# Kernel optimization log

Measured on AMD Instinct MI355X. Metric: run time of the kernel, lower is better.

## Reference

```python
import jax, jax.numpy as jnp
import numpy as np

EMBED_DIM = 512
NUM_HEADS = 8
HEAD_DIM = EMBED_DIM // NUM_HEADS
EDGE_HIDDEN = 512
B, L = 2, 512


def setup_inputs() -> dict:
    key = jax.random.key(0)
    ks = jax.random.split(key, 16)
    s = 0.02
    inp = {
        "query": jax.random.normal(ks[0], (B, L, EMBED_DIM), jnp.float32),
        "key_in": jax.random.normal(ks[1], (B, L, EMBED_DIM), jnp.float32),
        "value": jax.random.normal(ks[2], (B, L, EMBED_DIM), jnp.float32),
        "edge_representation": jax.random.normal(ks[3], (B, L, L), jnp.float32),
        # projection weights stored as [in, out]: y = x @ W + b
        "Wq": jax.random.normal(ks[4], (EMBED_DIM, EMBED_DIM), jnp.float32) * s,
        "bq": jnp.zeros((EMBED_DIM,), jnp.float32),
        "Wk": jax.random.normal(ks[5], (EMBED_DIM, EMBED_DIM), jnp.float32) * s,
        "bk": jnp.zeros((EMBED_DIM,), jnp.float32),
        "Wv": jax.random.normal(ks[6], (EMBED_DIM, EMBED_DIM), jnp.float32) * s,
        "bv": jnp.zeros((EMBED_DIM,), jnp.float32),
        "Wo": jax.random.normal(ks[7], (EMBED_DIM, EMBED_DIM), jnp.float32) * s,
        "bo": jnp.zeros((EMBED_DIM,), jnp.float32),
        # edge MLP: Linear(1 -> 512) -> ReLU -> Linear(512 -> num_heads)
        "We1": jax.random.normal(ks[8], (1, EDGE_HIDDEN), jnp.float32) * s,
        "be1": jnp.zeros((EDGE_HIDDEN,), jnp.float32),
        "We2": jax.random.normal(ks[9], (EDGE_HIDDEN, NUM_HEADS), jnp.float32) * s,
        "be2": jnp.zeros((NUM_HEADS,), jnp.float32),
    }
    return inp


def reference(query, key_in, value, edge_representation,
              Wq, bq, Wk, bk, Wv, bv, Wo, bo, We1, be1, We2, be2):
    Bc, Lc, _ = query.shape
    # project and split heads: [B, H, L, Dh]
    def split_heads(x):
        return x.reshape(Bc, Lc, NUM_HEADS, HEAD_DIM).transpose(0, 2, 1, 3)
    Q = split_heads(query @ Wq + bq)
    K = split_heads(key_in @ Wk + bk)
    V = split_heads(value @ Wv + bv)
    # edge MLP on scalar edge features: [B, L, L, 1] -> [B, L, L, H]
    e = edge_representation[..., None]
    h = jax.nn.relu(e * We1[0] + be1)          # [B, L, L, 512]
    edge_bias = h @ We2 + be2                   # [B, L, L, H]
    scale = 1.0 / jnp.sqrt(jnp.asarray(HEAD_DIM, query.dtype))
    scores = jnp.einsum("bhqd,bhkd->bhqk", Q, K) * scale
    scores = scores + edge_bias.transpose(0, 3, 1, 2)  # [B, H, L, L]
    attn = jax.nn.softmax(scores, axis=-1)
    out = jnp.einsum("bhqk,bhkd->bhqd", attn, V)
    out = out.transpose(0, 2, 1, 3).reshape(Bc, Lc, EMBED_DIM)
    return out @ Wo + bo
```

## Files before the change

kernel.cpp:

```cpp
#include <hip/hip_runtime.h>
#include <hip/hip_bf16.h>

typedef __attribute__((ext_vector_type(8))) short bf16x8;
typedef __attribute__((ext_vector_type(4))) float f32x4;

#define LOG2E 1.44269504088896340736f

#define XQ_OFF 0
#define XK_OFF 524288
#define XV_OFF 1048576
#define WQ_OFF 1572864
#define WK_OFF 1835008
#define WV_OFF 2097152
#define WO_OFF 2359296
#define QB_OFF 2621440
#define KB_OFF 3145728
#define VT_OFF 3670016
#define AO_OFF 4194304
#define T_B   9437184
#define A_B   (T_B + 4096)
#define C_B   (A_B + 20480)
#define SEG_B (C_B + 20480)

struct MegaArgs {
  const float *xq, *xk, *xv, *eg;
  const float *wq, *wk, *wv, *wo;
  const float *bq, *bk, *bv, *bo;
  const float *w1, *b1, *we2, *be2;
  float* out;
  unsigned short* wsb;
  float *wsT, *wsA, *wsC;
  unsigned short* segp;
};

__device__ __forceinline__ unsigned short f2bf(float f) {
  union { __hip_bfloat16 h; unsigned short u; } c;
  c.h = __float2bfloat16(f);
  return c.u;
}

__device__ void prep_block(const MegaArgs& a, char* smem) {
  float* sT   = (float*)smem;
  int*   sIdx = (int*)(smem + 2048);
  float (*sDA)[8] = (float (*)[8])(smem + 4096);
  float (*sDC)[8] = (float (*)[8])(smem + 20480);
  float* sA0 = (float*)(smem + 36864);
  float* sC0 = (float*)(smem + 36896);
  int tid = threadIdx.x;
  for (int p = tid; p < 512; p += 256) {
    float w = a.w1[p], bb = a.b1[p];
    sT[p] = (w != 0.f) ? (-bb / w) : -3.4e38f;
    sIdx[p] = p;
#pragma unroll
    for (int h = 0; h < 8; ++h) {
      float w2 = a.we2[p * 8 + h];
      float ra = 0.f, rc = 0.f;
      if (w < 0.f)       { ra = w2 * w; rc = w2 * bb; }
      else if (w == 0.f) { rc = w2 * fmaxf(bb, 0.f); }
      sDA[p][h] = ra; sDC[p][h] = rc;
    }
  }
  __syncthreads();
  for (int size = 2; size <= 512; size <<= 1) {
    for (int stride = size >> 1; stride > 0; stride >>= 1) {
      int p = tid;
      int i = ((p / stride) * (stride << 1)) + (p % stride);
      int j = i + stride;
      bool up = ((i & size) == 0);
      float ti = sT[i], tj = sT[j];
      if (up ? (ti > tj) : (ti < tj)) {
        sT[i] = tj; sT[j] = ti;
        int t = sIdx[i]; sIdx[i] = sIdx[j]; sIdx[j] = t;
      }
      __syncthreads();
    }
  }
#pragma unroll
  for (int h = 0; h < 8; ++h) { sDA[tid][h] += sDA[tid + 256][h]; sDC[tid][h] += sDC[tid + 256][h]; }
  __syncthreads();
  for (int st = 128; st > 0; st >>= 1) {
    if (tid < st) {
#pragma unroll
      for (int h = 0; h < 8; ++h) { sDA[tid][h] += sDA[tid + st][h]; sDC[tid][h] += sDC[tid + st][h]; }
    }
    __syncthreads();
  }
  if (tid < 8) { sA0[tid] = sDA[0][tid]; sC0[tid] = sDC[0][tid] + a.be2[tid]; }
  __syncthreads();
  for (int p = tid; p < 512; p += 256) {
    int k = sIdx[p];
    float wk = a.w1[k], bk2 = a.b1[k];
#pragma unroll
    for (int h = 0; h < 8; ++h) {
      float w2 = a.we2[k * 8 + h];
      float da = 0.f, dc = 0.f;
      if (wk > 0.f)      { da =  w2 * wk; dc =  w2 * bk2; }
      else if (wk < 0.f) { da = -w2 * wk; dc = -w2 * bk2; }
      sDA[p][h] = da; sDC[p][h] = dc;
    }
  }
  __syncthreads();
  for (int off = 1; off < 512; off <<= 1) {
    float ra[2][8], rc[2][8];
#pragma unroll
    for (int e = 0; e < 2; ++e) {
      int p = tid + e * 256;
      if (p >= off) {
#pragma unroll
        for (int h = 0; h < 8; ++h) { ra[e][h] = sDA[p - off][h]; rc[e][h] = sDC[p - off][h]; }
      }
    }
    __syncthreads();
#pragma unroll
    for (int e = 0; e < 2; ++e) {
      int p = tid + e * 256;
      if (p >= off) {
#pragma unroll
        for (int h = 0; h < 8; ++h) { sDA[p][h] += ra[e][h]; sDC[p][h] += rc[e][h]; }
      }
    }
    __syncthreads();
  }
  a.wsT[tid] = sT[tid]; a.wsT[tid + 256] = sT[tid + 256];
  if (tid < 8) { a.wsA[tid] = sA0[tid]; a.wsC[tid] = sC0[tid]; }
  for (int p = tid; p < 512; p += 256) {
#pragma unroll
    for (int h = 0; h < 8; ++h) {
      a.wsA[(p + 1) * 8 + h] = sA0[h] + sDA[p][h];
      a.wsC[(p + 1) * 8 + h] = sC0[h] + sDC[p][h];
    }
  }
}

__device__ void transpose2(const MegaArgs& a, int tblk, char* smem) {
  unsigned short (*sWt)[72] = (unsigned short (*)[72])smem;
  int tid = threadIdx.x;
  for (int it = 0; it < 2; ++it) {
    int t = tblk * 2 + it;
    int mat = t >> 6, tile = t & 63;
    int k0 = (tile >> 3) * 64, n0 = (tile & 7) * 64;
    const float* src = (mat == 0) ? a.wq : (mat == 1) ? a.wk : (mat == 2) ? a.wv : a.wo;
    int row = tid >> 2, cq = tid & 3;
    const float4* sp = (const float4*)(src + (size_t)(k0 + row) * 512 + n0 + cq * 16);
    if (it) __syncthreads();
#pragma unroll
    for (int j2 = 0; j2 < 4; ++j2) {
      float4 v = sp[j2];
      int nl = cq * 16 + j2 * 4;
      sWt[nl + 0][row] = f2bf(v.x);
      sWt[nl + 1][row] = f2bf(v.y);
      sWt[nl + 2][row] = f2bf(v.z);
      sWt[nl + 3][row] = f2bf(v.w);
    }
    __syncthreads();
    int n = tid >> 2, kq = tid & 3;
    unsigned short* dst = a.wsb + WQ_OFF + mat * 262144 + (size_t)(n0 + n) * 512 + k0 + kq * 16;
    *(uint4*)dst       = *(const uint4*)&sWt[n][kq * 16];
    *(uint4*)(dst + 8) = *(const uint4*)&sWt[n][kq * 16 + 8];
  }
}

__device__ void convert_units(const MegaArgs& a, int blk) {
  int tid = threadIdx.x;
  for (int u = blk - 129; u < 1536; u += 383) {
    int i = u * 256 + tid;
    int region = i >> 17, off = i & 131071;
    const float* src = (region == 0) ? a.xq : (region == 1) ? a.xk : a.xv;
    float4 v = ((const float4*)src)[off];
    ushort4 o;
    o.x = f2bf(v.x); o.y = f2bf(v.y); o.z = f2bf(v.z); o.w = f2bf(v.w);
    ((ushort4*)a.wsb)[i] = o;
  }
}

__device__ void seg_block(const MegaArgs& a, int sblk, char* smem) {
  float* sT = (float*)smem;
  int tid = threadIdx.x;
  sT[tid] = a.wsT[tid]; sT[tid + 256] = a.wsT[tid + 256];
  __syncthreads();
  int base = sblk * 4096;
  for (int j2 = 0; j2 < 16; ++j2) {
    int i = base + j2 * 256 + tid;
    float ev = a.eg[i];
    int lo = 0, hi = 512;
    while (lo < hi) {
      int mid = (lo + hi) >> 1;
      if (sT[mid] < ev) lo = mid + 1; else hi = mid;
    }
    a.segp[i] = (unsigned short)lo;
  }
}

__device__ void gemm_tile(const unsigned short* __restrict__ A, const unsigned short* __restrict__ Wt,
                          const float* __restrict__ bias, void* out, int mode,
                          int m0, int n0, char* smem) {
  const int K = 512;
  unsigned short (*sA)[72]  = (unsigned short (*)[72])smem;
  unsigned short (*sBt)[72] = (unsigned short (*)[72])(smem + 9216);
  int tid = threadIdx.x, wave = tid >> 6, lane = tid & 63;
  int quad = lane >> 4, l16 = lane & 15;
  f32x4 acc[4] = {{0.f,0.f,0.f,0.f},{0.f,0.f,0.f,0.f},{0.f,0.f,0.f,0.f},{0.f,0.f,0.f,0.f}};
  int lr = tid >> 2, ls = tid & 3;
  for (int kb = 0; kb < K; kb += 64) {
    __syncthreads();
    *(uint4*)&sA[lr][ls * 16]      = *(const uint4*)(A  + (size_t)(m0 + lr) * K + kb + ls * 16);
    *(uint4*)&sA[lr][ls * 16 + 8]  = *(const uint4*)(A  + (size_t)(m0 + lr) * K + kb + ls * 16 + 8);
    *(uint4*)&sBt[lr][ls * 16]     = *(const uint4*)(Wt + (size_t)(n0 + lr) * K + kb + ls * 16);
    *(uint4*)&sBt[lr][ls * 16 + 8] = *(const uint4*)(Wt + (size_t)(n0 + lr) * K + kb + ls * 16 + 8);
    __syncthreads();
    for (int ks = 0; ks < 2; ++ks) {
      bf16x8 af = *(const bf16x8*)&sA[wave * 16 + l16][ks * 32 + quad * 8];
#pragma unroll
      for (int nt = 0; nt < 4; ++nt) {
        bf16x8 bf = *(const bf16x8*)&sBt[nt * 16 + l16][ks * 32 + quad * 8];
        acc[nt] = __builtin_amdgcn_mfma_f32_16x16x32_bf16(af, bf, acc[nt], 0, 0, 0);
      }
    }
  }
  int mbase = m0 + wave * 16 + quad * 4;
#pragma unroll
  for (int nt = 0; nt < 4; ++nt) {
    int n = n0 + nt * 16 + l16;
    float bv = bias[n];
#pragma unroll
    for (int r = 0; r < 4; ++r) {
      float v = acc[nt][r] + bv;
      int m = mbase + r;
      if (mode == 0) {
        int b = m >> 9, l = m & 511, hh = n >> 6, d = n & 63;
        ((unsigned short*)out)[(((size_t)(b * 8 + hh) * 512) + l) * 64 + d] = f2bf(v);
      } else if (mode == 1) {
        ((float*)out)[(size_t)m * 512 + n] = v;
      } else {
        int b = m >> 9, l = m & 511, hh = n >> 6, d = n & 63;
        ((unsigned short*)out)[(((size_t)(b * 8 + hh) * 64) + d) * 512 + l] = f2bf(v);
      }
    }
  }
}

__device__ void attn_block(const MegaArgs& a, int qt, int h, int b, char* smem) {
  float* sAh = (float*)smem;
  float* sCh = (float*)(smem + 2052);
  unsigned short (*sP)[16][40] = (unsigned short (*)[16][40])(smem + 4112);
  float (*sO)[4][16][16] = (float (*)[4][16][16])(smem + 9232);
  float (*sM)[16] = (float (*)[16])(smem + 25616);
  float (*sL)[16] = (float (*)[16])(smem + 25872);
  const unsigned short* Qb = a.wsb + QB_OFF;
  const unsigned short* Kb = a.wsb + KB_OFF;
  const unsigned short* Vt = a.wsb + VT_OFF;
  int bh = b * 8 + h;
  int q0 = qt * 16;
  int tid = threadIdx.x, wave = tid >> 6, lane = tid & 63;
  int quad = lane >> 4, l16 = lane & 15;
  for (int i = tid; i < 513; i += 256) { sAh[i] = a.wsA[i * 8 + h]; sCh[i] = a.wsC[i * 8 + h]; }
  const unsigned short* qp = Qb + ((size_t)bh * 512 + q0 + l16) * 64 + quad * 8;
  bf16x8 qf0 = *(const bf16x8*)qp;
  bf16x8 qf1 = *(const bf16x8*)(qp + 32);
  int key_base = wave * 128;
  f32x4 S[4][2];
#pragma unroll
  for (int kt = 0; kt < 4; ++kt) {
    int key0 = key_base + kt * 32;
#pragma unroll
    for (int half = 0; half < 2; ++half) {
      const unsigned short* kp = Kb + ((size_t)bh * 512 + key0 + half * 16 + l16) * 64 + quad * 8;
      bf16x8 kf0 = *(const bf16x8*)kp;
      bf16x8 kf1 = *(const bf16x8*)(kp + 32);
      f32x4 acc = {0.f, 0.f, 0.f, 0.f};
      acc = __builtin_amdgcn_mfma_f32_16x16x32_bf16(qf0, kf0, acc, 0, 0, 0);
      acc = __builtin_amdgcn_mfma_f32_16x16x32_bf16(qf1, kf1, acc, 0, 0, 0);
      S[kt][half] = acc;
    }
  }
  __syncthreads();
#pragma unroll
  for (int kt = 0; kt < 4; ++kt)
#pragma unroll
    for (int half = 0; half < 2; ++half)
#pragma unroll
      for (int r = 0; r < 4; ++r) {
        int eidx = (b * 512 + q0 + quad * 4 + r) * 512 + key_base + kt * 32 + half * 16 + l16;
        float ev = a.eg[eidx];
        int sg = a.segp[eidx];
        S[kt][half][r] = S[kt][half][r] * 0.125f + sAh[sg] * ev + sCh[sg];
      }
  float m_w[4], l_w[4];
#pragma unroll
  for (int r = 0; r < 4; ++r) {
    float mx = -3.4e38f;
#pragma unroll
    for (int kt = 0; kt < 4; ++kt) { mx = fmaxf(mx, fmaxf(S[kt][0][r], S[kt][1][r])); }
    for (int off = 1; off < 16; off <<= 1) mx = fmaxf(mx, __shfl_xor(mx, off, 64));
    float s = 0.f;
#pragma unroll
    for (int kt = 0; kt < 4; ++kt)
#pragma unroll
      for (int half = 0; half < 2; ++half) {
        float p = exp2f((S[kt][half][r] - mx) * LOG2E);
        S[kt][half][r] = p; s += p;
      }
    for (int off = 1; off < 16; off <<= 1) s += __shfl_xor(s, off, 64);
    m_w[r] = mx; l_w[r] = s;
  }
  f32x4 Oacc[4] = {{0.f,0.f,0.f,0.f},{0.f,0.f,0.f,0.f},{0.f,0.f,0.f,0.f},{0.f,0.f,0.f,0.f}};
#pragma unroll
  for (int kt = 0; kt < 4; ++kt) {
    int key0 = key_base + kt * 32;
#pragma unroll
    for (int half = 0; half < 2; ++half)
#pragma unroll
      for (int r = 0; r < 4; ++r)
        sP[wave][quad * 4 + r][half * 16 + l16] = f2bf(S[kt][half][r]);
    __builtin_amdgcn_wave_barrier();
    bf16x8 pf = *(const bf16x8*)&sP[wave][l16][quad * 8];
    __builtin_amdgcn_wave_barrier();
#pragma unroll
    for (int nt = 0; nt < 4; ++nt) {
      bf16x8 vf = *(const bf16x8*)(Vt + ((size_t)bh * 64 + nt * 16 + l16) * 512 + key0 + quad * 8);
      Oacc[nt] = __builtin_amdgcn_mfma_f32_16x16x32_bf16(pf, vf, Oacc[nt], 0, 0, 0);
    }
  }
  if (l16 == 0) {
#pragma unroll
    for (int r = 0; r < 4; ++r) { sM[wave][quad * 4 + r] = m_w[r]; sL[wave][quad * 4 + r] = l_w[r]; }
  }
#pragma unroll
  for (int nt = 0; nt < 4; ++nt)
#pragma unroll
    for (int r = 0; r < 4; ++r)
      sO[wave][nt][quad * 4 + r][l16] = Oacc[nt][r];
  __syncthreads();
#pragma unroll
  for (int r = 0; r < 4; ++r) {
    int row = quad * 4 + r;
    float M = fmaxf(fmaxf(sM[0][row], sM[1][row]), fmaxf(sM[2][row], sM[3][row]));
    float L = 0.f, Ov = 0.f;
#pragma unroll
    for (int wv = 0; wv < 4; ++wv) {
      float f = exp2f((sM[wv][row] - M) * LOG2E);
      L += f * sL[wv][row];
      Ov += f * sO[wv][wave][row][l16];
    }
    float v = Ov / L;
    (a.wsb + AO_OFF)[((size_t)(b * 512 + q0 + row)) * 512 + h * 64 + wave * 16 + l16] = f2bf(v);
  }
}

__global__ __launch_bounds__(256) void k_pre(MegaArgs a) {
  __shared__ __align__(16) char smem[36928];
  int blk = blockIdx.x;
  if (blk == 0) prep_block(a, smem);
  else if (blk <= 128) transpose2(a, blk - 1, smem);
  else convert_units(a, blk);
}

__global__ __launch_bounds__(256) void k_qkv(MegaArgs a) {
  __shared__ __align__(16) char smem[18432];
  int blk = blockIdx.x;
  if (blk < 384) {
    int z = blk >> 7, rem = blk & 127;
    const unsigned short* A  = a.wsb + ((z == 0) ? XQ_OFF : (z == 1) ? XK_OFF : XV_OFF);
    const unsigned short* Wt = a.wsb + ((z == 0) ? WQ_OFF : (z == 1) ? WK_OFF : WV_OFF);
    const float* bias = (z == 0) ? a.bq : (z == 1) ? a.bk : a.bv;
    void* outp = (void*)(a.wsb + ((z == 0) ? QB_OFF : (z == 1) ? KB_OFF : VT_OFF));
    gemm_tile(A, Wt, bias, outp, (z == 2) ? 2 : 0, (rem & 15) * 64, (rem >> 4) * 64, smem);
  } else {
    seg_block(a, blk - 384, smem);
  }
}

__global__ __launch_bounds__(256) void k_at(MegaArgs a) {
  __shared__ __align__(16) char smem[26128];
  int blk = blockIdx.x;
  attn_block(a, blk & 31, (blk >> 5) & 7, blk >> 8, smem);
}

__global__ __launch_bounds__(256) void k_og(MegaArgs a) {
  __shared__ __align__(16) char smem[18432];
  gemm_tile(a.wsb + AO_OFF, a.wsb + WO_OFF, a.bo, (void*)a.out, 1,
            (blockIdx.x & 15) * 64, (blockIdx.x >> 4) * 64, smem);
}

extern "C" void kernel_launch(void* const* d_in, const int* in_sizes, int n_in,
                              void* d_out, int out_size, void* d_ws, size_t ws_size,
                              hipStream_t stream) {
  MegaArgs a;
  a.xq  = (const float*)d_in[0];
  a.xk  = (const float*)d_in[1];
  a.xv  = (const float*)d_in[2];
  a.eg  = (const float*)d_in[3];
  a.wq  = (const float*)d_in[4];
  a.bq  = (const float*)d_in[5];
  a.wk  = (const float*)d_in[6];
  a.bk  = (const float*)d_in[7];
  a.wv  = (const float*)d_in[8];
  a.bv  = (const float*)d_in[9];
  a.wo  = (const float*)d_in[10];
  a.bo  = (const float*)d_in[11];
  a.w1  = (const float*)d_in[12];
  a.b1  = (const float*)d_in[13];
  a.we2 = (const float*)d_in[14];
  a.be2 = (const float*)d_in[15];
  a.out = (float*)d_out;
  a.wsb = (unsigned short*)d_ws;
  a.wsT = (float*)((char*)d_ws + T_B);
  a.wsA = (float*)((char*)d_ws + A_B);
  a.wsC = (float*)((char*)d_ws + C_B);
  a.segp = (unsigned short*)((char*)d_ws + SEG_B);

  k_pre<<<512, 256, 0, stream>>>(a);
  k_qkv<<<512, 256, 0, stream>>>(a);
  k_at<<<512, 256, 0, stream>>>(a);
  k_og<<<128, 256, 0, stream>>>(a);
}
```

Baseline: 156.1 us.

## Spread conversion and segment search over more blocks; head-major prefix tables

The input bf16 conversion now runs one unit per block over 1536 extra blocks instead of a strided loop over 383 blocks, and the edge segment binary search uses 512 blocks of 1024 elements with a fixed 9-step branchless search instead of 128 blocks of 4096 elements. The per-head prefix tables wsA/wsC are stored head-major, so attention blocks read them contiguously instead of with a stride of 8. The aim is better latency hiding and occupancy in the pre and qkv kernels, and coalesced table loads. The cost is more block launch and scheduling overhead.

Measured after the change: 141.8 us. 1.1x faster.

```diff
diff --git a/kernel.cpp b/kernel.cpp
--- a/kernel.cpp
+++ b/kernel.cpp
@@ -122,12 +122,12 @@
     __syncthreads();
   }
   a.wsT[tid] = sT[tid]; a.wsT[tid + 256] = sT[tid + 256];
-  if (tid < 8) { a.wsA[tid] = sA0[tid]; a.wsC[tid] = sC0[tid]; }
+  if (tid < 8) { a.wsA[tid * 513] = sA0[tid]; a.wsC[tid * 513] = sC0[tid]; }
   for (int p = tid; p < 512; p += 256) {
 #pragma unroll
     for (int h = 0; h < 8; ++h) {
-      a.wsA[(p + 1) * 8 + h] = sA0[h] + sDA[p][h];
-      a.wsC[(p + 1) * 8 + h] = sC0[h] + sDC[p][h];
+      a.wsA[h * 513 + p + 1] = sA0[h] + sDA[p][h];
+      a.wsC[h * 513 + p + 1] = sC0[h] + sDC[p][h];
     }
   }
 }
@@ -160,35 +160,30 @@
   }
 }
 
-__device__ void convert_units(const MegaArgs& a, int blk) {
-  int tid = threadIdx.x;
-  for (int u = blk - 129; u < 1536; u += 383) {
-    int i = u * 256 + tid;
-    int region = i >> 17, off = i & 131071;
-    const float* src = (region == 0) ? a.xq : (region == 1) ? a.xk : a.xv;
-    float4 v = ((const float4*)src)[off];
-    ushort4 o;
-    o.x = f2bf(v.x); o.y = f2bf(v.y); o.z = f2bf(v.z); o.w = f2bf(v.w);
-    ((ushort4*)a.wsb)[i] = o;
-  }
-}
-
 __device__ void seg_block(const MegaArgs& a, int sblk, char* smem) {
   float* sT = (float*)smem;
   int tid = threadIdx.x;
   sT[tid] = a.wsT[tid]; sT[tid + 256] = a.wsT[tid + 256];
   __syncthreads();
-  int base = sblk * 4096;
-  for (int j2 = 0; j2 < 16; ++j2) {
-    int i = base + j2 * 256 + tid;
-    float ev = a.eg[i];
+  int base = sblk * 1024;
+  float ev[4];
+#pragma unroll
+  for (int j = 0; j < 4; ++j) ev[j] = a.eg[base + j * 256 + tid];
+  int res[4];
+#pragma unroll
+  for (int j = 0; j < 4; ++j) {
     int lo = 0, hi = 512;
-    while (lo < hi) {
+#pragma unroll
+    for (int it = 0; it < 9; ++it) {
       int mid = (lo + hi) >> 1;
-      if (sT[mid] < ev) lo = mid + 1; else hi = mid;
-    }
-    a.segp[i] = (unsigned short)lo;
-  }
+      bool c = sT[mid] < ev[j];
+      lo = c ? mid + 1 : lo;
+      hi = c ? hi : mid;
+    }
+    res[j] = lo;
+  }
+#pragma unroll
+  for (int j = 0; j < 4; ++j) a.segp[base + j * 256 + tid] = (unsigned short)res[j];
 }
 
 __device__ void gemm_tile(const unsigned short* __restrict__ A, const unsigned short* __restrict__ Wt,
@@ -253,7 +248,7 @@
   int q0 = qt * 16;
   int tid = threadIdx.x, wave = tid >> 6, lane = tid & 63;
   int quad = lane >> 4, l16 = lane & 15;
-  for (int i = tid; i < 513; i += 256) { sAh[i] = a.wsA[i * 8 + h]; sCh[i] = a.wsC[i * 8 + h]; }
+  for (int i = tid; i < 513; i += 256) { sAh[i] = a.wsA[h * 513 + i]; sCh[i] = a.wsC[h * 513 + i]; }
   const unsigned short* qp = Qb + ((size_t)bh * 512 + q0 + l16) * 64 + quad * 8;
   bf16x8 qf0 = *(const bf16x8*)qp;
   bf16x8 qf1 = *(const bf16x8*)(qp + 32);
@@ -352,7 +347,15 @@
   int blk = blockIdx.x;
   if (blk == 0) prep_block(a, smem);
   else if (blk <= 128) transpose2(a, blk - 1, smem);
-  else convert_units(a, blk);
+  else {
+    int i = (blk - 129) * 256 + threadIdx.x;
+    int region = i >> 17, off = i & 131071;
+    const float* src = (region == 0) ? a.xq : (region == 1) ? a.xk : a.xv;
+    float4 v = ((const float4*)src)[off];
+    ushort4 o;
+    o.x = f2bf(v.x); o.y = f2bf(v.y); o.z = f2bf(v.z); o.w = f2bf(v.w);
+    ((ushort4*)a.wsb)[i] = o;
+  }
 }
 
 __global__ __launch_bounds__(256) void k_qkv(MegaArgs a) {
@@ -409,8 +412,8 @@
   a.wsC = (float*)((char*)d_ws + C_B);
   a.segp = (unsigned short*)((char*)d_ws + SEG_B);
 
-  k_pre<<<512, 256, 0, stream>>>(a);
-  k_qkv<<<512, 256, 0, stream>>>(a);
+  k_pre<<<1665, 256, 0, stream>>>(a);
+  k_qkv<<<896, 256, 0, stream>>>(a);
   k_at<<<512, 256, 0, stream>>>(a);
   k_og<<<128, 256, 0, stream>>>(a);
 }
```
